# Kernel optimization log

Hardware: AMD Instinct MI355X
Metric: run time of the kernel (lower is better)

## Reference

```python
import jax, jax.numpy as jnp
import numpy as np

N_NODES = 200000
N_EDGES = 400000
N_GRAPHS = 4096
H = 300
L = 5
BN_EPS = 1e-5


def setup_inputs() -> dict:
    key = jax.random.key(0)
    ks = jax.random.split(key, 12)
    s = 0.05  # weight scale for numerical stability across 5 layers
    return {
        'x': jax.random.randint(ks[0], (N_NODES, 9), 0, 120),
        'edge_index': jax.random.randint(ks[1], (2, N_EDGES), 0, N_NODES),
        'edge_attr': jax.random.randint(ks[2], (N_EDGES, 3), 0, 16),
        'batch': jnp.sort(jax.random.randint(ks[3], (N_NODES,), 0, N_GRAPHS)),
        'atom_emb': jax.random.normal(ks[4], (9, 120, H), jnp.float32) * s,
        'bond_emb': jax.random.normal(ks[5], (L, 3, 16, H), jnp.float32) * s,
        'eps': jnp.zeros((L,), jnp.float32),
        'W1': jax.random.normal(ks[6], (L, H, 2 * H), jnp.float32) * s,
        'b1': jnp.zeros((L, 2 * H), jnp.float32),
        'bn_gamma': jnp.ones((L, 2 * H), jnp.float32),
        'bn_beta': jnp.zeros((L, 2 * H), jnp.float32),
        'bn_mean': jnp.zeros((L, 2 * H), jnp.float32),
        'bn_var': jnp.ones((L, 2 * H), jnp.float32),
        'W2': jax.random.normal(ks[7], (L, 2 * H, H), jnp.float32) * s,
        'b2': jnp.zeros((L, H), jnp.float32),
        'cls_W': jax.random.normal(ks[8], (H, 2), jnp.float32) * s,
        'cls_b': jnp.zeros((2,), jnp.float32),
    }


def reference(x, edge_index, edge_attr, batch, atom_emb, bond_emb, eps,
              W1, b1, bn_gamma, bn_beta, bn_mean, bn_var, W2, b2, cls_W, cls_b):
    N = x.shape[0]
    # AtomEncoder: sum of 9 categorical embeddings -> [N, H]
    h = jnp.sum(atom_emb[jnp.arange(9)[None, :], x], axis=1)
    src, dst = edge_index[0], edge_index[1]
    feat_idx3 = jnp.arange(3)[None, :]
    for l in range(W1.shape[0]):
        # BondEncoder for this layer: sum of 3 categorical embeddings -> [E, H]
        e = jnp.sum(bond_emb[l][feat_idx3, edge_attr], axis=1)
        # message = relu(x_j + edge_emb), aggregated by scatter-add at dst
        m = jax.nn.relu(h[src] + e)
        agg = jax.ops.segment_sum(m, dst, num_segments=N)
        z = (1.0 + eps[l]) * h + agg
        # MLP: Linear(H,2H) -> BN(eval) -> ReLU -> Linear(2H,H)
        z = z @ W1[l] + b1[l]
        z = (z - bn_mean[l]) * (bn_gamma[l] * jax.lax.rsqrt(bn_var[l] + BN_EPS)) + bn_beta[l]
        z = jax.nn.relu(z)
        h = z @ W2[l] + b2[l]
    # global mean pool over graphs
    sums = jax.ops.segment_sum(h, batch, num_segments=N_GRAPHS)
    counts = jax.ops.segment_sum(jnp.ones((N, 1), h.dtype), batch, num_segments=N_GRAPHS)
    graph_feature = sums / jnp.maximum(counts, 1.0)
    logits = graph_feature @ cls_W + cls_b
    return logits, graph_feature
```

## Files before the change

### kernel.cpp

```cpp
#include <hip/hip_runtime.h>
#include <hip/hip_bf16.h>

#define N_NODES 200000
#define N_EDGES 400000
#define N_GRAPHS 4096
#define HDIM 300
#define H2DIM 600
#define NLAYERS 5

typedef __hip_bfloat16 bf16;
typedef __attribute__((ext_vector_type(4))) short s16x4;
typedef __attribute__((ext_vector_type(8))) short s16x8;
typedef __attribute__((ext_vector_type(4))) float f32x4v;

__device__ inline short f2bf(float f) {
    __hip_bfloat16 b = __float2bfloat16(f);
    return *(short*)&b;
}
__device__ inline float bf2f(short s) {
    __hip_bfloat16 b = *(__hip_bfloat16*)&s;
    return __bfloat162float(b);
}

__device__ inline void gload_lds16(const short* g, short* l) {
    __builtin_amdgcn_global_load_lds(
        (const __attribute__((address_space(1))) unsigned int*)g,
        (__attribute__((address_space(3))) unsigned int*)l,
        16, 0, 0);
}

__global__ void diag_kernel(float* __restrict__ out, int n, float val) {
    int i = blockIdx.x * blockDim.x + threadIdx.x;
    if (i < n) out[i] = val;
}

__global__ void hist_kernel(const int* __restrict__ edge_index, int* __restrict__ offs) {
    int e = blockIdx.x * blockDim.x + threadIdx.x;
    if (e >= N_EDGES) return;
    atomicAdd(&offs[edge_index[N_EDGES + e]], 1);
}

#define SCAN_N 200001
__global__ void scan1_kernel(int* __restrict__ offs, int* __restrict__ bsum) {
    __shared__ int ls[256];
    int tid = threadIdx.x;
    int base = blockIdx.x * 1024 + tid * 4;
    int v[4];
#pragma unroll
    for (int j = 0; j < 4; j++) v[j] = (base + j < SCAN_N) ? offs[base + j] : 0;
    int t = v[0] + v[1] + v[2] + v[3];
    ls[tid] = t;
    __syncthreads();
    for (int off = 1; off < 256; off <<= 1) {
        int y = (tid >= off) ? ls[tid - off] : 0;
        __syncthreads();
        ls[tid] += y;
        __syncthreads();
    }
    int ex = ls[tid] - t;
#pragma unroll
    for (int j = 0; j < 4; j++) {
        if (base + j < SCAN_N) offs[base + j] = ex;
        ex += v[j];
    }
    if (tid == 255) bsum[blockIdx.x] = ls[255];
}

__global__ void scan2_kernel(int* __restrict__ bsum, int nb) {
    __shared__ int ls[256];
    int tid = threadIdx.x;
    int v = (tid < nb) ? bsum[tid] : 0;
    ls[tid] = v;
    __syncthreads();
    for (int off = 1; off < 256; off <<= 1) {
        int y = (tid >= off) ? ls[tid - off] : 0;
        __syncthreads();
        ls[tid] += y;
        __syncthreads();
    }
    if (tid < nb) bsum[tid] = ls[tid] - v;
}

__global__ void scan3_kernel(int* __restrict__ offs, const int* __restrict__ bsum) {
    int i = blockIdx.x * blockDim.x + threadIdx.x;
    if (i >= SCAN_N) return;
    offs[i] += bsum[i >> 10];
}

__global__ void scatter_kernel(const int* __restrict__ edge_index,
                               const int* __restrict__ edge_attr,
                               int* __restrict__ offs,
                               int* __restrict__ sidx) {
    int e = blockIdx.x * blockDim.x + threadIdx.x;
    if (e >= N_EDGES) return;
    int src = edge_index[e];
    int dst = edge_index[N_EDGES + e];
    int combo = edge_attr[e * 3 + 0] | (edge_attr[e * 3 + 1] << 4) | (edge_attr[e * 3 + 2] << 8);
    int pos = atomicAdd(&offs[dst], 1);
    sidx[pos] = src | (combo << 18);
}

__global__ void etab_kernel(const float* __restrict__ bond_l, short* __restrict__ etab) {
    int idx = blockIdx.x * blockDim.x + threadIdx.x;
    if (idx >= 4096 * 304) return;
    int combo = idx / 304;
    int c = idx - combo * 304;
    if (c >= HDIM) { etab[idx] = 0; return; }
    int a0 = combo & 15, a1 = (combo >> 4) & 15, a2 = combo >> 8;
    float v = bond_l[a0 * HDIM + c] + bond_l[16 * HDIM + a1 * HDIM + c]
            + bond_l[32 * HDIM + a2 * HDIM + c];
    etab[idx] = f2bf(v);
}

__global__ void prep_w_swz(const float* __restrict__ W1, const float* __restrict__ W2,
                           short* __restrict__ Wt1s, short* __restrict__ Wt2s) {
    int idx = blockIdx.x * blockDim.x + threadIdx.x;
    const int G1 = NLAYERS * 40 * 10 * 64;
    const int G2 = NLAYERS * 20 * 20 * 64;
    if (idx < G1) {
        int l = idx / (40 * 10 * 64);
        int r = idx - l * (40 * 10 * 64);
        int nt = r / (10 * 64);
        int r2 = r - nt * (10 * 64);
        int kb = r2 >> 6;
        int lane = r2 & 63;
        int n = nt * 16 + (lane & 15);
        int k0 = kb * 32 + (lane >> 4) * 8;
        s16x8 o;
#pragma unroll
        for (int j = 0; j < 8; j++) {
            int k = k0 + j;
            float v = (n < H2DIM && k < HDIM) ? W1[((size_t)l * HDIM + k) * H2DIM + n] : 0.f;
            o[j] = f2bf(v);
        }
        *(s16x8*)&Wt1s[(size_t)idx * 8] = o;
    } else if (idx < G1 + G2) {
        int t = idx - G1;
        int l = t / (20 * 20 * 64);
        int r = t - l * (20 * 20 * 64);
        int nt = r / (20 * 64);
        int r2 = r - nt * (20 * 64);
        int kb = r2 >> 6;
        int lane = r2 & 63;
        int n = nt * 16 + (lane & 15);
        int k0 = kb * 32 + (lane >> 4) * 8;
        s16x8 o;
#pragma unroll
        for (int j = 0; j < 8; j++) {
            int k = k0 + j;
            float v = (n < HDIM && k < H2DIM) ? W2[((size_t)l * H2DIM + k) * HDIM + n] : 0.f;
            o[j] = f2bf(v);
        }
        *(s16x8*)&Wt2s[(size_t)t * 8] = o;
    }
}

__global__ void atom_kernel(const int* __restrict__ x,
                            const float* __restrict__ atom_emb,
                            short* __restrict__ h) {
    int i = blockIdx.x * blockDim.x + threadIdx.x;
    if (i >= N_NODES * 75) return;
    int n = i / 75;
    int c = (i - n * 75) * 4;
    const int* xr = x + n * 9;
    float4 s = {0.f, 0.f, 0.f, 0.f};
#pragma unroll
    for (int f = 0; f < 9; f++) {
        float4 v = *(const float4*)&atom_emb[(size_t)(f * 120 + xr[f]) * HDIM + c];
        s.x += v.x; s.y += v.y; s.z += v.z; s.w += v.w;
    }
    s16x4 o = {f2bf(s.x), f2bf(s.y), f2bf(s.z), f2bf(s.w)};
    *(s16x4*)&h[(size_t)n * HDIM + c] = o;
}

__launch_bounds__(256)
__global__ void agg_kernel(const short* __restrict__ h_in,
                           short* __restrict__ z,
                           const int* __restrict__ offs,
                           const int* __restrict__ sidx,
                           const short* __restrict__ etab,
                           const float* __restrict__ eps, int l) {
    int tid = threadIdx.x;
    int q = tid >> 4;
    int l16 = tid & 15;
    int n = blockIdx.x * 16 + q;
    float e1 = 1.f + eps[l];
    int beg = (n == 0) ? 0 : offs[n - 1];
    int end = offs[n];

    float4 acc[5];
#pragma unroll
    for (int j = 0; j < 5; j++) acc[j] = (float4){0.f, 0.f, 0.f, 0.f};
    bool tail = l16 < 11;
    int ctail = 256 + l16 * 4;

    int e = beg;
    for (; e + 2 <= end; e += 2) {
        int pk0 = sidx[e];
        int pk1 = sidx[e + 1];
        const short* hr0 = h_in + (size_t)(pk0 & 0x3FFFF) * HDIM;
        const short* er0 = etab + (((unsigned)pk0) >> 18) * 304;
        const short* hr1 = h_in + (size_t)(pk1 & 0x3FFFF) * HDIM;
        const short* er1 = etab + (((unsigned)pk1) >> 18) * 304;
        s16x4 hv0[5], ev0[5], hv1[5], ev1[5];
#pragma unroll
        for (int rep = 0; rep < 4; rep++) {
            int c = rep * 64 + l16 * 4;
            hv0[rep] = *(const s16x4*)(hr0 + c);
            ev0[rep] = *(const s16x4*)(er0 + c);
            hv1[rep] = *(const s16x4*)(hr1 + c);
            ev1[rep] = *(const s16x4*)(er1 + c);
        }
        if (tail) {
            hv0[4] = *(const s16x4*)(hr0 + ctail);
            ev0[4] = *(const s16x4*)(er0 + ctail);
            hv1[4] = *(const s16x4*)(hr1 + ctail);
            ev1[4] = *(const s16x4*)(er1 + ctail);
        }
#pragma unroll
        for (int rep = 0; rep < 5; rep++) {
            if (rep == 4 && !tail) continue;
            acc[rep].x += fmaxf(0.f, bf2f(hv0[rep].x) + bf2f(ev0[rep].x))
                        + fmaxf(0.f, bf2f(hv1[rep].x) + bf2f(ev1[rep].x));
            acc[rep].y += fmaxf(0.f, bf2f(hv0[rep].y) + bf2f(ev0[rep].y))
                        + fmaxf(0.f, bf2f(hv1[rep].y) + bf2f(ev1[rep].y));
            acc[rep].z += fmaxf(0.f, bf2f(hv0[rep].z) + bf2f(ev0[rep].z))
                        + fmaxf(0.f, bf2f(hv1[rep].z) + bf2f(ev1[rep].z));
            acc[rep].w += fmaxf(0.f, bf2f(hv0[rep].w) + bf2f(ev0[rep].w))
                        + fmaxf(0.f, bf2f(hv1[rep].w) + bf2f(ev1[rep].w));
        }
    }
    if (e < end) {
        int pk0 = sidx[e];
        const short* hr0 = h_in + (size_t)(pk0 & 0x3FFFF) * HDIM;
        const short* er0 = etab + (((unsigned)pk0) >> 18) * 304;
        s16x4 hv0[5], ev0[5];
#pragma unroll
        for (int rep = 0; rep < 4; rep++) {
            int c = rep * 64 + l16 * 4;
            hv0[rep] = *(const s16x4*)(hr0 + c);
            ev0[rep] = *(const s16x4*)(er0 + c);
        }
        if (tail) {
            hv0[4] = *(const s16x4*)(hr0 + ctail);
            ev0[4] = *(const s16x4*)(er0 + ctail);
        }
#pragma unroll
        for (int rep = 0; rep < 5; rep++) {
            if (rep == 4 && !tail) continue;
            acc[rep].x += fmaxf(0.f, bf2f(hv0[rep].x) + bf2f(ev0[rep].x));
            acc[rep].y += fmaxf(0.f, bf2f(hv0[rep].y) + bf2f(ev0[rep].y));
            acc[rep].z += fmaxf(0.f, bf2f(hv0[rep].z) + bf2f(ev0[rep].z));
            acc[rep].w += fmaxf(0.f, bf2f(hv0[rep].w) + bf2f(ev0[rep].w));
        }
    }

    const short* hn = h_in + (size_t)n * HDIM;
    short* zr = z + (size_t)n * HDIM;
#pragma unroll
    for (int rep = 0; rep < 5; rep++) {
        if (rep == 4 && !tail) continue;
        int c = rep < 4 ? rep * 64 + l16 * 4 : ctail;
        s16x4 hv = *(const s16x4*)(hn + c);
        s16x4 o;
        o.x = f2bf(fmaf(e1, bf2f(hv.x), acc[rep].x));
        o.y = f2bf(fmaf(e1, bf2f(hv.y), acc[rep].y));
        o.z = f2bf(fmaf(e1, bf2f(hv.z), acc[rep].z));
        o.w = f2bf(fmaf(e1, bf2f(hv.w), acc[rep].w));
        *(s16x4*)(zr + c) = o;
    }
}

#define ZST 328
#define WBUF_OFF (64 * ZST)
#define WBUF_SHORTS (20 * 64 * 8)
#define YS_OFF (WBUF_OFF + WBUF_SHORTS)
#define YST 136
#define LDS_SHORTS (YS_OFF + 64 * YST)

__launch_bounds__(256, 2)
__global__ void mlp_kernel(const short* __restrict__ zin,
                           short* __restrict__ hout,
                           const short* __restrict__ Wt1,
                           const short* __restrict__ Wt2,
                           const float* __restrict__ b1l,
                           const float* __restrict__ gammal,
                           const float* __restrict__ betal,
                           const float* __restrict__ meanl,
                           const float* __restrict__ varl,
                           const float* __restrict__ b2l) {
    __shared__ short lds[LDS_SHORTS];
    int tid = threadIdx.x;
    int wng = tid >> 6;
    int lane = tid & 63;
    int quad = lane >> 4;
    int l16 = lane & 15;
    int row0 = blockIdx.x * 64;

    for (int i = tid; i < 64 * 82; i += 256) {
        int r = i / 82;
        int p = (i - r * 82) * 4;
        s16x4 v = *(const s16x4*)&zin[(size_t)(row0 + r) * HDIM + p];
        *(s16x4*)&lds[r * ZST + p] = v;
    }

    f32x4v acc2[4][5];
#pragma unroll
    for (int rt = 0; rt < 4; rt++)
#pragma unroll
        for (int ct = 0; ct < 5; ct++) acc2[rt][ct] = (f32x4v){0.f, 0.f, 0.f, 0.f};

    for (int cc = 0; cc < 5; cc++) {
        f32x4v acc1[4][2];
#pragma unroll
        for (int rt = 0; rt < 4; rt++)
#pragma unroll
            for (int ct = 0; ct < 2; ct++) acc1[rt][ct] = (f32x4v){0.f, 0.f, 0.f, 0.f};

        for (int kbp = 0; kbp < 5; kbp++) {
            __syncthreads();
#pragma unroll
            for (int j = 0; j < 4; j++) {
                int c = j * 4 + wng;
                int nt_ = c >> 1, kb2 = c & 1;
                const short* src = Wt1 +
                    ((size_t)(((cc * 8 + nt_) * 10 + kbp * 2 + kb2) * 64) + lane) * 8;
                gload_lds16(src, &lds[WBUF_OFF + c * 512]);
            }
            __syncthreads();
#pragma unroll
            for (int kb2 = 0; kb2 < 2; kb2++) {
                int ks = (kbp * 2 + kb2) * 32 + quad * 8;
                s16x8 a[4];
#pragma unroll
                for (int rt = 0; rt < 4; rt++)
                    a[rt] = *(const s16x8*)&lds[(rt * 16 + l16) * ZST + ks];
#pragma unroll
                for (int ct = 0; ct < 2; ct++) {
                    int c = (wng * 2 + ct) * 2 + kb2;
                    s16x8 b = *(const s16x8*)&lds[WBUF_OFF + c * 512 + lane * 8];
#pragma unroll
                    for (int rt = 0; rt < 4; rt++)
                        acc1[rt][ct] = __builtin_amdgcn_mfma_f32_16x16x32_bf16(a[rt], b, acc1[rt][ct], 0, 0, 0);
                }
            }
        }
#pragma unroll
        for (int ct = 0; ct < 2; ct++) {
            int kc = wng * 32 + ct * 16 + l16;
            int col = cc * 128 + kc;
            bool valid = col < H2DIM;
            float s = 0.f, sh = 0.f;
            if (valid) {
                s = gammal[col] * rsqrtf(varl[col] + 1e-5f);
                sh = betal[col] + (b1l[col] - meanl[col]) * s;
            }
#pragma unroll
            for (int rt = 0; rt < 4; rt++)
#pragma unroll
                for (int rr = 0; rr < 4; rr++) {
                    float v = valid ? fmaxf(0.f, fmaf(acc1[rt][ct][rr], s, sh)) : 0.f;
                    lds[YS_OFF + (rt * 16 + quad * 4 + rr) * YST + kc] = f2bf(v);
                }
        }
#pragma unroll
        for (int kbl = 0; kbl < 4; kbl++) {
            __syncthreads();
#pragma unroll
            for (int j = 0; j < 5; j++) {
                int c = j * 4 + wng;
                const short* src = Wt2 +
                    ((size_t)((c * 20 + cc * 4 + kbl) * 64) + lane) * 8;
                gload_lds16(src, &lds[WBUF_OFF + c * 512]);
            }
            __syncthreads();
            int ks = kbl * 32 + quad * 8;
            s16x8 a[4];
#pragma unroll
            for (int rt = 0; rt < 4; rt++)
                a[rt] = *(const s16x8*)&lds[YS_OFF + (rt * 16 + l16) * YST + ks];
#pragma unroll
            for (int ct = 0; ct < 5; ct++) {
                int c = wng * 5 + ct;
                s16x8 b = *(const s16x8*)&lds[WBUF_OFF + c * 512 + lane * 8];
#pragma unroll
                for (int rt = 0; rt < 4; rt++)
                    acc2[rt][ct] = __builtin_amdgcn_mfma_f32_16x16x32_bf16(a[rt], b, acc2[rt][ct], 0, 0, 0);
            }
        }
    }
#pragma unroll
    for (int ct = 0; ct < 5; ct++) {
        int col = wng * 80 + ct * 16 + l16;
        if (col < HDIM) {
            float bb = b2l[col];
#pragma unroll
            for (int rt = 0; rt < 4; rt++)
#pragma unroll
                for (int rr = 0; rr < 4; rr++) {
                    int r = rt * 16 + quad * 4 + rr;
                    lds[r * HDIM + col] = f2bf(acc2[rt][ct][rr] + bb);
                }
        }
    }
    __syncthreads();
    for (int i = tid; i < 64 * 75; i += 256) {
        *(s16x4*)&hout[(size_t)row0 * HDIM + i * 4] = *(const s16x4*)&lds[i * 4];
    }
}

__device__ int lower_bound_dev(const int* a, int n, int v) {
    int lo = 0, hi = n;
    while (lo < hi) {
        int mid = (lo + hi) >> 1;
        if (a[mid] < v) lo = mid + 1; else hi = mid;
    }
    return lo;
}

__global__ void pool_kernel(const short* __restrict__ h,
                            const int* __restrict__ batch,
                            const float* __restrict__ cls_W,
                            const float* __restrict__ cls_b,
                            float* __restrict__ out) {
    __shared__ int seg[2];
    __shared__ float r0s[256], r1s[256];
    int g = blockIdx.x;
    int t = threadIdx.x;
    if (t == 0) {
        seg[0] = lower_bound_dev(batch, N_NODES, g);
        seg[1] = lower_bound_dev(batch, N_NODES, g + 1);
    }
    __syncthreads();
    int s = seg[0], e = seg[1];
    float inv = 1.f / fmaxf((float)(e - s), 1.f);
    float p0 = 0.f, p1 = 0.f;
    if (t < 75) {
        int c = t * 4;
        float4 sum = {0.f, 0.f, 0.f, 0.f};
        for (int n = s; n < e; n++) {
            s16x4 v = *(const s16x4*)&h[(size_t)n * HDIM + c];
            sum.x += bf2f(v.x);
            sum.y += bf2f(v.y);
            sum.z += bf2f(v.z);
            sum.w += bf2f(v.w);
        }
        float4 gf = {sum.x * inv, sum.y * inv, sum.z * inv, sum.w * inv};
        *(float4*)&out[2 * N_GRAPHS + (size_t)g * HDIM + c] = gf;
        p0 = gf.x * cls_W[c * 2] + gf.y * cls_W[(c + 1) * 2]
           + gf.z * cls_W[(c + 2) * 2] + gf.w * cls_W[(c + 3) * 2];
        p1 = gf.x * cls_W[c * 2 + 1] + gf.y * cls_W[(c + 1) * 2 + 1]
           + gf.z * cls_W[(c + 2) * 2 + 1] + gf.w * cls_W[(c + 3) * 2 + 1];
    }
    r0s[t] = p0;
    r1s[t] = p1;
    __syncthreads();
    for (int st = 128; st > 0; st >>= 1) {
        if (t < st) { r0s[t] += r0s[t + st]; r1s[t] += r1s[t + st]; }
        __syncthreads();
    }
    if (t == 0) {
        out[g * 2 + 0] = r0s[0] + cls_b[0];
        out[g * 2 + 1] = r1s[0] + cls_b[1];
    }
}

extern "C" void kernel_launch(void* const* d_in, const int* in_sizes, int n_in,
                              void* d_out, int out_size, void* d_ws, size_t ws_size,
                              hipStream_t stream) {
    const int* x          = (const int*)d_in[0];
    const int* edge_index = (const int*)d_in[1];
    const int* edge_attr  = (const int*)d_in[2];
    const int* batch      = (const int*)d_in[3];
    const float* atom_emb = (const float*)d_in[4];
    const float* bond_emb = (const float*)d_in[5];
    const float* eps      = (const float*)d_in[6];
    const float* W1       = (const float*)d_in[7];
    const float* b1       = (const float*)d_in[8];
    const float* bn_gamma = (const float*)d_in[9];
    const float* bn_beta  = (const float*)d_in[10];
    const float* bn_mean  = (const float*)d_in[11];
    const float* bn_var   = (const float*)d_in[12];
    const float* W2       = (const float*)d_in[13];
    const float* b2       = (const float*)d_in[14];
    const float* cls_W    = (const float*)d_in[15];
    const float* cls_b    = (const float*)d_in[16];
    float* out = (float*)d_out;

    char* base = (char*)d_ws;
    const size_t OFF_HA   = 0;
    const size_t OFF_HB   = 120000000;
    const size_t OFF_WT1  = 240000000;
    const size_t OFF_WT2  = 242048000;
    const size_t OFF_ETAB = 244096000;
    const size_t OFF_SIDX = 246586368;
    const size_t OFF_OFFS = 248186368;
    const size_t OFF_BSUM = 248986384;
    const size_t TOTAL    = 248987168;

    if (ws_size < TOTAL) {
        float mb = (float)(ws_size >> 20);
        diag_kernel<<<(out_size + 255) / 256, 256, 0, stream>>>(out, out_size, mb);
        return;
    }

    short* hA   = (short*)(base + OFF_HA);
    short* hB   = (short*)(base + OFF_HB);
    short* Wt1s = (short*)(base + OFF_WT1);
    short* Wt2s = (short*)(base + OFF_WT2);
    short* etab = (short*)(base + OFF_ETAB);
    int*   sidx = (int*)(base + OFF_SIDX);
    int*   offs = (int*)(base + OFF_OFFS);
    int*   bsum = (int*)(base + OFF_BSUM);

    hipMemsetAsync(offs, 0, SCAN_N * sizeof(int), stream);
    hist_kernel<<<(N_EDGES + 255) / 256, 256, 0, stream>>>(edge_index, offs);
    scan1_kernel<<<196, 256, 0, stream>>>(offs, bsum);
    scan2_kernel<<<1, 256, 0, stream>>>(bsum, 196);
    scan3_kernel<<<(SCAN_N + 255) / 256, 256, 0, stream>>>(offs, bsum);
    scatter_kernel<<<(N_EDGES + 255) / 256, 256, 0, stream>>>(edge_index, edge_attr, offs, sidx);

    {
        int total = NLAYERS * 40 * 10 * 64 + NLAYERS * 20 * 20 * 64;
        prep_w_swz<<<(total + 255) / 256, 256, 0, stream>>>(W1, W2, Wt1s, Wt2s);
    }
    atom_kernel<<<(N_NODES * 75 + 255) / 256, 256, 0, stream>>>(x, atom_emb, hA);

    for (int l = 0; l < NLAYERS; l++) {
        etab_kernel<<<(4096 * 304 + 255) / 256, 256, 0, stream>>>(
            bond_emb + (size_t)l * 3 * 16 * HDIM, etab);
        agg_kernel<<<N_NODES / 16, 256, 0, stream>>>(
            hA, hB, offs, sidx, etab, eps, l);
        mlp_kernel<<<N_NODES / 64, 256, 0, stream>>>(
            hB, hA,
            Wt1s + (size_t)l * 640 * 320, Wt2s + (size_t)l * 320 * 640,
            b1 + l * H2DIM, bn_gamma + l * H2DIM, bn_beta + l * H2DIM,
            bn_mean + l * H2DIM, bn_var + l * H2DIM, b2 + l * HDIM);
    }

    pool_kernel<<<N_GRAPHS, 256, 0, stream>>>(hA, batch, cls_W, cls_b, out);
}
```

Before: 2.424 ms.

## Software-pipeline MLP kernel weight loads with register fragments and swizzled LDS

Flattens the two nested GEMM loops of the MLP kernel into one 45-step loop. Each step reads its A/B fragments into registers, then issues the next weight tile's global-to-LDS copy so it overlaps the current MFMAs. The padded z tile in LDS is replaced by an XOR-swizzled layout with stride 320 to avoid bank conflicts, and MFMA phases get raised wave priority. It keeps one LDS weight buffer and a barrier per step, and holds more fragment registers, which could limit occupancy.

```diff
diff --git a/kernel.cpp b/kernel.cpp
--- a/kernel.cpp
+++ b/kernel.cpp
@@ -271,8 +271,8 @@
     }
 }
 
-#define ZST 328
-#define WBUF_OFF (64 * ZST)
+#define ZSTRIDE 320
+#define WBUF_OFF (64 * ZSTRIDE)
 #define WBUF_SHORTS (20 * 64 * 8)
 #define YS_OFF (WBUF_OFF + WBUF_SHORTS)
 #define YST 136
@@ -297,98 +297,160 @@
     int l16 = lane & 15;
     int row0 = blockIdx.x * 64;
 
-    for (int i = tid; i < 64 * 82; i += 256) {
-        int r = i / 82;
-        int p = (i - r * 82) * 4;
-        s16x4 v = *(const s16x4*)&zin[(size_t)(row0 + r) * HDIM + p];
-        *(s16x4*)&lds[r * ZST + p] = v;
-    }
-
+#pragma unroll
+    for (int j = 0; j < 4; j++) {
+        int sub = j * 4 + wng;
+        int nt_ = sub >> 1, kb2 = sub & 1;
+        const short* src = Wt1 + ((size_t)((nt_ * 10 + kb2) * 64) + lane) * 8;
+        gload_lds16(src, &lds[WBUF_OFF + sub * 512]);
+    }
+
+    {
+        const short* zbase = zin + (size_t)row0 * HDIM;
+        for (int i = tid; i < 64 * 40; i += 256) {
+            int r = i / 40;
+            int cs = i - r * 40;
+            const short* srcp = zbase + r * HDIM + cs * 8;
+            s16x4 v0 = *(const s16x4*)srcp;
+            s16x4 v1 = *(const s16x4*)(srcp + 4);
+            int d = r * ZSTRIDE + ((cs ^ (r & 7)) << 3);
+            *(s16x4*)&lds[d] = v0;
+            *(s16x4*)&lds[d + 4] = v1;
+        }
+    }
+
+    f32x4v acc1[4][2];
     f32x4v acc2[4][5];
 #pragma unroll
-    for (int rt = 0; rt < 4; rt++)
+    for (int rt = 0; rt < 4; rt++) {
+#pragma unroll
+        for (int ct = 0; ct < 2; ct++) acc1[rt][ct] = (f32x4v){0.f, 0.f, 0.f, 0.f};
 #pragma unroll
         for (int ct = 0; ct < 5; ct++) acc2[rt][ct] = (f32x4v){0.f, 0.f, 0.f, 0.f};
-
-    for (int cc = 0; cc < 5; cc++) {
-        f32x4v acc1[4][2];
+    }
+
+    s16x8 fa[8], fb[5];
+
+    __syncthreads();
+
+#pragma unroll
+    for (int kb2 = 0; kb2 < 2; kb2++) {
+        int ks = kb2 * 32 + quad * 8;
 #pragma unroll
         for (int rt = 0; rt < 4; rt++)
-#pragma unroll
-            for (int ct = 0; ct < 2; ct++) acc1[rt][ct] = (f32x4v){0.f, 0.f, 0.f, 0.f};
-
-        for (int kbp = 0; kbp < 5; kbp++) {
-            __syncthreads();
-#pragma unroll
-            for (int j = 0; j < 4; j++) {
-                int c = j * 4 + wng;
-                int nt_ = c >> 1, kb2 = c & 1;
-                const short* src = Wt1 +
-                    ((size_t)(((cc * 8 + nt_) * 10 + kbp * 2 + kb2) * 64) + lane) * 8;
-                gload_lds16(src, &lds[WBUF_OFF + c * 512]);
-            }
-            __syncthreads();
-#pragma unroll
-            for (int kb2 = 0; kb2 < 2; kb2++) {
-                int ks = (kbp * 2 + kb2) * 32 + quad * 8;
-                s16x8 a[4];
-#pragma unroll
-                for (int rt = 0; rt < 4; rt++)
-                    a[rt] = *(const s16x8*)&lds[(rt * 16 + l16) * ZST + ks];
-#pragma unroll
-                for (int ct = 0; ct < 2; ct++) {
-                    int c = (wng * 2 + ct) * 2 + kb2;
-                    s16x8 b = *(const s16x8*)&lds[WBUF_OFF + c * 512 + lane * 8];
-#pragma unroll
-                    for (int rt = 0; rt < 4; rt++)
-                        acc1[rt][ct] = __builtin_amdgcn_mfma_f32_16x16x32_bf16(a[rt], b, acc1[rt][ct], 0, 0, 0);
+            fa[kb2 * 4 + rt] = *(const s16x8*)&lds[(rt * 16 + l16) * ZSTRIDE
+                                                   + (ks ^ ((l16 & 7) << 3))];
+#pragma unroll
+        for (int ct = 0; ct < 2; ct++)
+            fb[kb2 * 2 + ct] = *(const s16x8*)&lds[WBUF_OFF
+                                                   + ((wng * 2 + ct) * 2 + kb2) * 512 + lane * 8];
+    }
+    __syncthreads();
+
+#pragma unroll 1
+    for (int c = 0; c < 45; c++) {
+        int cc = c / 9;
+        int r = c - cc * 9;
+        int cn = c + 1;
+        if (cn < 45) {
+            int ccn = cn / 9;
+            int rn = cn - ccn * 9;
+            if (rn < 5) {
+#pragma unroll
+                for (int j = 0; j < 4; j++) {
+                    int sub = j * 4 + wng;
+                    int nt_ = sub >> 1, kb2 = sub & 1;
+                    const short* src = Wt1 +
+                        ((size_t)(((ccn * 8 + nt_) * 10 + rn * 2 + kb2) * 64) + lane) * 8;
+                    gload_lds16(src, &lds[WBUF_OFF + sub * 512]);
+                }
+            } else {
+                int kbl = rn - 5;
+#pragma unroll
+                for (int j = 0; j < 5; j++) {
+                    int sub = j * 4 + wng;
+                    const short* src = Wt2 +
+                        ((size_t)((sub * 20 + ccn * 4 + kbl) * 64) + lane) * 8;
+                    gload_lds16(src, &lds[WBUF_OFF + sub * 512]);
                 }
             }
         }
-#pragma unroll
-        for (int ct = 0; ct < 2; ct++) {
-            int kc = wng * 32 + ct * 16 + l16;
-            int col = cc * 128 + kc;
-            bool valid = col < H2DIM;
-            float s = 0.f, sh = 0.f;
-            if (valid) {
-                s = gammal[col] * rsqrtf(varl[col] + 1e-5f);
-                sh = betal[col] + (b1l[col] - meanl[col]) * s;
+        __builtin_amdgcn_sched_barrier(0);
+        __builtin_amdgcn_s_setprio(1);
+        if (r < 5) {
+#pragma unroll
+            for (int kb2 = 0; kb2 < 2; kb2++)
+#pragma unroll
+                for (int ct = 0; ct < 2; ct++)
+#pragma unroll
+                    for (int rt = 0; rt < 4; rt++)
+                        acc1[rt][ct] = __builtin_amdgcn_mfma_f32_16x16x32_bf16(
+                            fa[kb2 * 4 + rt], fb[kb2 * 2 + ct], acc1[rt][ct], 0, 0, 0);
+        } else {
+#pragma unroll
+            for (int ct = 0; ct < 5; ct++)
+#pragma unroll
+                for (int rt = 0; rt < 4; rt++)
+                    acc2[rt][ct] = __builtin_amdgcn_mfma_f32_16x16x32_bf16(
+                        fa[rt], fb[ct], acc2[rt][ct], 0, 0, 0);
+        }
+        __builtin_amdgcn_s_setprio(0);
+        if (r == 4) {
+#pragma unroll
+            for (int ct = 0; ct < 2; ct++) {
+                int kc = wng * 32 + ct * 16 + l16;
+                int col = cc * 128 + kc;
+                bool valid = col < H2DIM;
+                float s = 0.f, sh = 0.f;
+                if (valid) {
+                    s = gammal[col] * rsqrtf(varl[col] + 1e-5f);
+                    sh = betal[col] + (b1l[col] - meanl[col]) * s;
+                }
+#pragma unroll
+                for (int rt = 0; rt < 4; rt++)
+#pragma unroll
+                    for (int rr = 0; rr < 4; rr++) {
+                        float v = valid ? fmaxf(0.f, fmaf(acc1[rt][ct][rr], s, sh)) : 0.f;
+                        lds[YS_OFF + (rt * 16 + quad * 4 + rr) * YST + kc] = f2bf(v);
+                    }
             }
 #pragma unroll
             for (int rt = 0; rt < 4; rt++)
 #pragma unroll
-                for (int rr = 0; rr < 4; rr++) {
-                    float v = valid ? fmaxf(0.f, fmaf(acc1[rt][ct][rr], s, sh)) : 0.f;
-                    lds[YS_OFF + (rt * 16 + quad * 4 + rr) * YST + kc] = f2bf(v);
+                for (int ct = 0; ct < 2; ct++) acc1[rt][ct] = (f32x4v){0.f, 0.f, 0.f, 0.f};
+        }
+        if (c == 44) break;
+        __builtin_amdgcn_sched_barrier(0);
+        __syncthreads();
+        {
+            int ccn = cn / 9;
+            int rn = cn - ccn * 9;
+            if (rn < 5) {
+#pragma unroll
+                for (int kb2 = 0; kb2 < 2; kb2++) {
+                    int ks = (rn * 2 + kb2) * 32 + quad * 8;
+#pragma unroll
+                    for (int rt = 0; rt < 4; rt++)
+                        fa[kb2 * 4 + rt] = *(const s16x8*)&lds[(rt * 16 + l16) * ZSTRIDE
+                                                               + (ks ^ ((l16 & 7) << 3))];
+#pragma unroll
+                    for (int ct = 0; ct < 2; ct++)
+                        fb[kb2 * 2 + ct] = *(const s16x8*)&lds[WBUF_OFF
+                                                               + ((wng * 2 + ct) * 2 + kb2) * 512 + lane * 8];
                 }
-        }
-#pragma unroll
-        for (int kbl = 0; kbl < 4; kbl++) {
-            __syncthreads();
-#pragma unroll
-            for (int j = 0; j < 5; j++) {
-                int c = j * 4 + wng;
-                const short* src = Wt2 +
-                    ((size_t)((c * 20 + cc * 4 + kbl) * 64) + lane) * 8;
-                gload_lds16(src, &lds[WBUF_OFF + c * 512]);
+            } else {
+                int ks = (rn - 5) * 32 + quad * 8;
+#pragma unroll
+                for (int rt = 0; rt < 4; rt++)
+                    fa[rt] = *(const s16x8*)&lds[YS_OFF + (rt * 16 + l16) * YST + ks];
+#pragma unroll
+                for (int ct = 0; ct < 5; ct++)
+                    fb[ct] = *(const s16x8*)&lds[WBUF_OFF + (wng * 5 + ct) * 512 + lane * 8];
             }
-            __syncthreads();
-            int ks = kbl * 32 + quad * 8;
-            s16x8 a[4];
-#pragma unroll
-            for (int rt = 0; rt < 4; rt++)
-                a[rt] = *(const s16x8*)&lds[YS_OFF + (rt * 16 + l16) * YST + ks];
-#pragma unroll
-            for (int ct = 0; ct < 5; ct++) {
-                int c = wng * 5 + ct;
-                s16x8 b = *(const s16x8*)&lds[WBUF_OFF + c * 512 + lane * 8];
-#pragma unroll
-                for (int rt = 0; rt < 4; rt++)
-                    acc2[rt][ct] = __builtin_amdgcn_mfma_f32_16x16x32_bf16(a[rt], b, acc2[rt][ct], 0, 0, 0);
-            }
-        }
-    }
+        }
+        __syncthreads();
+    }
+
 #pragma unroll
     for (int ct = 0; ct < 5; ct++) {
         int col = wng * 80 + ct * 16 + l16;
@@ -398,8 +460,8 @@
             for (int rt = 0; rt < 4; rt++)
 #pragma unroll
                 for (int rr = 0; rr < 4; rr++) {
-                    int r = rt * 16 + quad * 4 + rr;
-                    lds[r * HDIM + col] = f2bf(acc2[rt][ct][rr] + bb);
+                    int rrow = rt * 16 + quad * 4 + rr;
+                    lds[rrow * HDIM + col] = f2bf(acc2[rt][ct][rr] + bb);
                 }
         }
     }
```

After: 4.456 ms. 1.84x slower.

## Load MLP weight fragments directly from global memory and swizzle Z tile in LDS

Applied to the files above, without the earlier changes.

The MLP kernel no longer stages W1/W2 fragments into LDS with global_load_lds and paired barriers. Each wave now reads its B fragments straight from global memory (L2-resident pre-swizzled weights), which removes most __syncthreads calls and frees LDS for occupancy. The Z tile is stored with an XOR swizzle at stride 320 to avoid LDS bank conflicts on A-fragment reads. The trade-off is that weight fragments are re-fetched per wave from global/L2 instead of being shared across the block, so global load latency is exposed directly in the MFMA loop.

```diff
diff --git a/kernel.cpp b/kernel.cpp
--- a/kernel.cpp
+++ b/kernel.cpp
@@ -20,13 +20,6 @@
 __device__ inline float bf2f(short s) {
     __hip_bfloat16 b = *(__hip_bfloat16*)&s;
     return __bfloat162float(b);
-}
-
-__device__ inline void gload_lds16(const short* g, short* l) {
-    __builtin_amdgcn_global_load_lds(
-        (const __attribute__((address_space(1))) unsigned int*)g,
-        (__attribute__((address_space(3))) unsigned int*)l,
-        16, 0, 0);
 }
 
 __global__ void diag_kernel(float* __restrict__ out, int n, float val) {
@@ -271,10 +264,8 @@
     }
 }
 
-#define ZST 328
-#define WBUF_OFF (64 * ZST)
-#define WBUF_SHORTS (20 * 64 * 8)
-#define YS_OFF (WBUF_OFF + WBUF_SHORTS)
+#define ZSTRIDE 320
+#define YS_OFF (64 * ZSTRIDE)
 #define YST 136
 #define LDS_SHORTS (YS_OFF + 64 * YST)
 
@@ -297,11 +288,18 @@
     int l16 = lane & 15;
     int row0 = blockIdx.x * 64;
 
-    for (int i = tid; i < 64 * 82; i += 256) {
-        int r = i / 82;
-        int p = (i - r * 82) * 4;
-        s16x4 v = *(const s16x4*)&zin[(size_t)(row0 + r) * HDIM + p];
-        *(s16x4*)&lds[r * ZST + p] = v;
+    {
+        const short* zbase = zin + (size_t)row0 * HDIM;
+        for (int i = tid; i < 64 * 40; i += 256) {
+            int r = i / 40;
+            int cs = i - r * 40;
+            const short* srcp = zbase + r * HDIM + cs * 8;
+            s16x4 v0 = *(const s16x4*)srcp;
+            s16x4 v1 = *(const s16x4*)(srcp + 4);
+            int d = r * ZSTRIDE + ((cs ^ (r & 7)) << 3);
+            *(s16x4*)&lds[d] = v0;
+            *(s16x4*)&lds[d + 4] = v1;
+        }
     }
 
     f32x4v acc2[4][5];
@@ -309,6 +307,8 @@
     for (int rt = 0; rt < 4; rt++)
 #pragma unroll
         for (int ct = 0; ct < 5; ct++) acc2[rt][ct] = (f32x4v){0.f, 0.f, 0.f, 0.f};
+
+    __syncthreads();
 
     for (int cc = 0; cc < 5; cc++) {
         f32x4v acc1[4][2];
@@ -317,34 +317,25 @@
 #pragma unroll
             for (int ct = 0; ct < 2; ct++) acc1[rt][ct] = (f32x4v){0.f, 0.f, 0.f, 0.f};
 
-        for (int kbp = 0; kbp < 5; kbp++) {
-            __syncthreads();
-#pragma unroll
-            for (int j = 0; j < 4; j++) {
-                int c = j * 4 + wng;
-                int nt_ = c >> 1, kb2 = c & 1;
-                const short* src = Wt1 +
-                    ((size_t)(((cc * 8 + nt_) * 10 + kbp * 2 + kb2) * 64) + lane) * 8;
-                gload_lds16(src, &lds[WBUF_OFF + c * 512]);
+#pragma unroll 2
+        for (int kb = 0; kb < 10; kb++) {
+            int ks = kb * 32 + quad * 8;
+            s16x8 a[4];
+#pragma unroll
+            for (int rt = 0; rt < 4; rt++)
+                a[rt] = *(const s16x8*)&lds[(rt * 16 + l16) * ZSTRIDE
+                                            + (ks ^ ((l16 & 7) << 3))];
+#pragma unroll
+            for (int ct = 0; ct < 2; ct++) {
+                s16x8 b = *(const s16x8*)&Wt1[
+                    ((size_t)(((cc * 8 + wng * 2 + ct) * 10 + kb) * 64) + lane) * 8];
+#pragma unroll
+                for (int rt = 0; rt < 4; rt++)
+                    acc1[rt][ct] = __builtin_amdgcn_mfma_f32_16x16x32_bf16(
+                        a[rt], b, acc1[rt][ct], 0, 0, 0);
             }
-            __syncthreads();
-#pragma unroll
-            for (int kb2 = 0; kb2 < 2; kb2++) {
-                int ks = (kbp * 2 + kb2) * 32 + quad * 8;
-                s16x8 a[4];
-#pragma unroll
-                for (int rt = 0; rt < 4; rt++)
-                    a[rt] = *(const s16x8*)&lds[(rt * 16 + l16) * ZST + ks];
-#pragma unroll
-                for (int ct = 0; ct < 2; ct++) {
-                    int c = (wng * 2 + ct) * 2 + kb2;
-                    s16x8 b = *(const s16x8*)&lds[WBUF_OFF + c * 512 + lane * 8];
-#pragma unroll
-                    for (int rt = 0; rt < 4; rt++)
-                        acc1[rt][ct] = __builtin_amdgcn_mfma_f32_16x16x32_bf16(a[rt], b, acc1[rt][ct], 0, 0, 0);
-                }
-            }
-        }
+        }
+        __syncthreads();
 #pragma unroll
         for (int ct = 0; ct < 2; ct++) {
             int kc = wng * 32 + ct * 16 + l16;
@@ -363,17 +354,9 @@
                     lds[YS_OFF + (rt * 16 + quad * 4 + rr) * YST + kc] = f2bf(v);
                 }
         }
-#pragma unroll
+        __syncthreads();
+#pragma unroll 2
         for (int kbl = 0; kbl < 4; kbl++) {
-            __syncthreads();
-#pragma unroll
-            for (int j = 0; j < 5; j++) {
-                int c = j * 4 + wng;
-                const short* src = Wt2 +
-                    ((size_t)((c * 20 + cc * 4 + kbl) * 64) + lane) * 8;
-                gload_lds16(src, &lds[WBUF_OFF + c * 512]);
-            }
-            __syncthreads();
             int ks = kbl * 32 + quad * 8;
             s16x8 a[4];
 #pragma unroll
@@ -381,14 +364,16 @@
                 a[rt] = *(const s16x8*)&lds[YS_OFF + (rt * 16 + l16) * YST + ks];
 #pragma unroll
             for (int ct = 0; ct < 5; ct++) {
-                int c = wng * 5 + ct;
-                s16x8 b = *(const s16x8*)&lds[WBUF_OFF + c * 512 + lane * 8];
+                s16x8 b = *(const s16x8*)&Wt2[
+                    ((size_t)(((wng * 5 + ct) * 20 + cc * 4 + kbl) * 64) + lane) * 8];
 #pragma unroll
                 for (int rt = 0; rt < 4; rt++)
-                    acc2[rt][ct] = __builtin_amdgcn_mfma_f32_16x16x32_bf16(a[rt], b, acc2[rt][ct], 0, 0, 0);
+                    acc2[rt][ct] = __builtin_amdgcn_mfma_f32_16x16x32_bf16(
+                        a[rt], b, acc2[rt][ct], 0, 0, 0);
             }
         }
     }
+
 #pragma unroll
     for (int ct = 0; ct < 5; ct++) {
         int col = wng * 80 + ct * 16 + l16;
@@ -398,8 +383,8 @@
             for (int rt = 0; rt < 4; rt++)
 #pragma unroll
                 for (int rr = 0; rr < 4; rr++) {
-                    int r = rt * 16 + quad * 4 + rr;
-                    lds[r * HDIM + col] = f2bf(acc2[rt][ct][rr] + bb);
+                    int rrow = rt * 16 + quad * 4 + rr;
+                    lds[rrow * HDIM + col] = f2bf(acc2[rt][ct][rr] + bb);
                 }
         }
     }
```

Result: slower. 2.719 ms (+12.2%).
